# Kernel optimization log

Hardware: AMD Instinct MI355X
Metric: run time of the kernel (lower is better)

## Reference

```python
import jax, jax.numpy as jnp
import numpy as np

A = 64        # atom_fea_len
NBR = 41      # nbr_fea_len
ORIG = 92     # orig_atom_fea_len
NCONV = 3
N = 50000     # total atoms
M = 12        # neighbors per atom
B = 1000      # crystals
NPC = 50      # atoms per crystal (B*NPC == N)
EPS = 1e-5


def setup_inputs() -> dict:
    key = jax.random.key(0)
    ks = jax.random.split(key, 16)
    s = lambda k, shape: (jax.random.normal(k, shape, jnp.float32) * 0.05)
    inp = {
        "atom_fea": jax.random.normal(ks[0], (N, ORIG), jnp.float32),
        "nbr_fea": jax.random.uniform(ks[1], (N, M, NBR), dtype=jnp.float32),
        "nbr_fea_idx": jax.random.randint(ks[2], (N, M), 0, N),
        "crystal_atom_idx": jnp.arange(B * NPC).reshape(B, NPC),
        # params (weights stored as (in, out) so fwd is x @ w + b)
        "emb_w": s(ks[3], (ORIG, A)),
        "fc_full_w": s(ks[4], (NCONV, 2 * A + NBR, 2 * A)),
        "fc_full_b": s(ks[5], (NCONV, 2 * A)),
        "bn1_g": jnp.ones((NCONV, 2 * A), jnp.float32),
        "bn1_b": jnp.zeros((NCONV, 2 * A), jnp.float32),
        "bn2_g": jnp.ones((NCONV, A), jnp.float32),
        "bn2_b": jnp.zeros((NCONV, A), jnp.float32),
        "adj_w": s(ks[6], (6, A, A)),   # torch Bilinear weight (out, in1, in2)
        "adj_b": s(ks[7], (6,)),
        "fc1_w": s(ks[8], (6, 6)),
        "fc1_b": s(ks[9], (6,)),
        "af_w": s(ks[10], (A, ORIG)),
        "af_b": s(ks[11], (ORIG,)),
    }
    return inp


def _batchnorm(x, g, b):
    # training-mode BN over axis 0 (torch default biased variance)
    m = jnp.mean(x, axis=0)
    v = jnp.var(x, axis=0)
    return (x - m) * jax.lax.rsqrt(v + EPS) * g + b


def _conv_layer(x, nbr_fea, nbr_idx, w, b, g1, b1, g2, b2):
    n, m = nbr_idx.shape
    atom_nbr = x[nbr_idx]  # (N, M, A) gather
    total = jnp.concatenate(
        [jnp.broadcast_to(x[:, None, :], (n, m, A)), atom_nbr, nbr_fea], axis=2
    )  # (N, M, 2A+NBR)
    gated = total @ w + b  # (N, M, 2A)
    gated = _batchnorm(gated.reshape(-1, 2 * A), g1, b1).reshape(n, m, 2 * A)
    nbr_filter, nbr_core = gated[..., :A], gated[..., A:]
    summed = jnp.sum(jax.nn.sigmoid(nbr_filter) * jax.nn.softplus(nbr_core), axis=1)
    summed = _batchnorm(summed, g2, b2)
    return jax.nn.softplus(x + summed)


def reference(atom_fea, nbr_fea, nbr_fea_idx, crystal_atom_idx, emb_w,
              fc_full_w, fc_full_b, bn1_g, bn1_b, bn2_g, bn2_b,
              adj_w, adj_b, fc1_w, fc1_b, af_w, af_b):
    x = atom_fea @ emb_w  # embedding, no bias
    for i in range(NCONV):
        x = _conv_layer(x, nbr_fea, nbr_fea_idx,
                        fc_full_w[i], fc_full_b[i],
                        bn1_g[i], bn1_b[i], bn2_g[i], bn2_b[i])
    cf = x[crystal_atom_idx]  # (B, NPC, A)
    # Original code bug: fc_adj(x1, x2) is called with x1 == x2 == tiled atom
    # features, so pair (i, j) depends only on atom j. Compute per-atom bilinear
    # then tile -> identical output.
    q = jnp.einsum('bnd,ode,bne->bno', cf, adj_w, cf) + adj_b  # (B, NPC, 6)
    q = q @ fc1_w + fc1_b
    logp = jax.nn.log_softmax(q, axis=-1)  # row-wise over the 6 classes
    edge_prob = jnp.broadcast_to(logp[:, None, :, :], (B, NPC, NPC, 6)).reshape(B, NPC * NPC, 6)
    atom_feature = cf @ af_w + af_b  # (B, NPC, ORIG)
    return edge_prob, atom_feature
```

## Files before the change

### kernel.cpp

```cpp
#include <hip/hip_runtime.h>
#include <hip/hip_bf16.h>

#define AA 64
#define NBRF 41
#define ORIGD 92
#define NATOM 50000
#define MM 12
#define NB 1000
#define NPCC 50
#define NEDGE (NATOM*MM)
#define NREP 64
constexpr float EPS_BN = 1e-5f;

using bf16 = __hip_bfloat16;
typedef short s16x8 __attribute__((ext_vector_type(8)));
typedef float f32x4 __attribute__((ext_vector_type(4)));

__device__ __forceinline__ float u2f(unsigned short u) {
    union { float f; unsigned int i; } v; v.i = ((unsigned int)u) << 16; return v.f;
}
__device__ __forceinline__ unsigned short f2bu(float f) {
    bf16 h = __float2bfloat16(f);
    return *reinterpret_cast<unsigned short*>(&h);
}
__device__ __forceinline__ float fsigmoid(float x) {
    float e = __expf(-x);
    return __builtin_amdgcn_rcpf(1.f + e);
}
__device__ __forceinline__ float fsoftplus(float x) {
    return fmaxf(x, 0.f) + __logf(1.f + __expf(-fabsf(x)));
}

#define GLD16(g, l)                                                              \
    __builtin_amdgcn_global_load_lds(                                            \
        (const __attribute__((address_space(1))) unsigned int*)(g),              \
        (__attribute__((address_space(3))) unsigned int*)(l), 16, 0, 0)

__global__ __launch_bounds__(256) void k_prepN(const float* __restrict__ nf,
                                               unsigned short* __restrict__ nbp) {
    const int total = NEDGE * 6;
    for (int i = blockIdx.x * 256 + threadIdx.x; i < total; i += gridDim.x * 256) {
        int row = i / 6, j = i - row * 6;
        const float* src = nf + (size_t)row * NBRF + j * 8;
        int base = j * 8;
        unsigned short h[8];
        #pragma unroll
        for (int e = 0; e < 8; ++e)
            h[e] = (base + e < NBRF) ? f2bu(src[e]) : (unsigned short)0;
        uint4 u;
        u.x = (unsigned)h[0] | ((unsigned)h[1] << 16);
        u.y = (unsigned)h[2] | ((unsigned)h[3] << 16);
        u.z = (unsigned)h[4] | ((unsigned)h[5] << 16);
        u.w = (unsigned)h[6] | ((unsigned)h[7] << 16);
        *reinterpret_cast<uint4*>(nbp + (size_t)row * 48 + j * 8) = u;
    }
}

__global__ void k_prepW(const float* __restrict__ W_all, unsigned short* __restrict__ WtAll,
                        const float* __restrict__ adjw, unsigned short* __restrict__ Bq,
                        float* __restrict__ stats, int nstat) {
    int b = blockIdx.x, t = threadIdx.x;
    if (b < 9) {
        int layer = b / 3, part = b - layer * 3;
        const float* W = W_all + (size_t)layer * 169 * 128;
        unsigned short* Wt = WtAll + layer * 27648 + part * 9216;
        for (int i = t; i < 9216; i += 256) {
            int n = i / 72, k = i - n * 72;
            float v = 0.f;
            if (part == 0)      { if (k < NBRF) v = W[(128 + k) * 128 + n]; }
            else if (part == 1) { if (k < 64)   v = W[(64 + k) * 128 + n]; }
            else                { if (k < 64)   v = W[k * 128 + n]; }
            Wt[i] = f2bu(v);
        }
    } else if (b < 12) {
        int base = (b - 9) * 9216;
        for (int i = t; i < 9216; i += 256) {
            int idx = base + i;
            int n = idx / 72, k = idx - n * 72;
            float v = (k < 64) ? adjw[(n >> 6) * 4096 + k * 64 + (n & 63)] : 0.f;
            Bq[idx] = f2bu(v);
        }
    } else {
        int base = (b - 12) * 2048;
        for (int i = t; i < 2048; i += 256) {
            int idx = base + i;
            if (idx < nstat) stats[idx] = 0.f;
        }
    }
}

__global__ __launch_bounds__(256) void k_embed(const float* __restrict__ af,
                                               const float* __restrict__ w,
                                               unsigned short* __restrict__ xb) {
    __shared__ float wl[ORIGD * AA];
    __shared__ float al[4][ORIGD];
    int t = threadIdx.x;
    for (int i = t; i < ORIGD * AA; i += 256) wl[i] = w[i];
    int n0 = blockIdx.x * 4;
    for (int i = t; i < 4 * ORIGD; i += 256) {
        int a = i / ORIGD, k = i - a * ORIGD;
        al[a][k] = af[(size_t)(n0 + a) * ORIGD + k];
    }
    __syncthreads();
    int c = t & 63, a = t >> 6;
    float acc = 0.f;
    #pragma unroll 4
    for (int k = 0; k < ORIGD; ++k)
        acc += al[a][k] * wl[k * AA + c];
    xb[(size_t)(n0 + a) * AA + c] = f2bu(acc);
}

__global__ __launch_bounds__(256, 2) void k_passA(const unsigned short* __restrict__ xb,
                                                  const unsigned short* __restrict__ nbp,
                                                  const unsigned short* __restrict__ Wt,
                                                  const int* __restrict__ nidx,
                                                  float* __restrict__ stats,
                                                  uint4* __restrict__ gated) {
    __shared__ __attribute__((aligned(16))) unsigned char SMEM[63488];
    unsigned short* A   = reinterpret_cast<unsigned short*>(SMEM);
    unsigned short* As  = A + 192 * 64;
    unsigned short* Bl0 = As + 16 * 64;
    unsigned short* Bl1 = Bl0 + 128 * 72;
    int t = threadIdx.x;
    int n0 = blockIdx.x * 16;
    int w = t >> 6, lane = t & 63, ln = lane & 15, quad = lane >> 4;

    const unsigned short* nbrow = nbp + (size_t)n0 * MM * 48;
    for (int c = w; c < 18; c += 4)
        GLD16(nbrow + c * 512 + lane * 8, (char*)A + c * 1024);
    for (int c = w; c < 18; c += 4)
        GLD16(Wt + c * 512 + lane * 8, (char*)Bl0 + c * 1024);
    for (int c = w; c < 18; c += 4)
        GLD16(Wt + 9216 + c * 512 + lane * 8, (char*)Bl1 + c * 1024);
    int sl = ((lane & 7) ^ ((lane >> 3) & 7)) * 8;
    if (w == 3) {
        GLD16(xb + (size_t)(n0 + (lane >> 3)) * 64 + sl, (char*)As);
        GLD16(xb + (size_t)(n0 + 8 + (lane >> 3)) * 64 + sl, (char*)As + 1024);
    }
    if (t < 64) A[192 * 48 + t] = 0;
    const int* nb = nidx + n0 * MM;
    int idxv[6];
    #pragma unroll
    for (int c = 0; c < 6; ++c) idxv[c] = nb[w * 48 + c * 8 + (lane >> 3)];
    __syncthreads();

    f32x4 acc[3][8];
    f32x4 z4 = {0.f, 0.f, 0.f, 0.f};
    for (int i = 0; i < 3; ++i) for (int j = 0; j < 8; ++j) acc[i][j] = z4;
    int sw0 = (quad ^ (ln & 7)) * 8, sw1 = ((quad + 4) ^ (ln & 7)) * 8;

    #pragma unroll
    for (int mt = 0; mt < 3; ++mt) {
        int mrow = w * 48 + mt * 16 + ln;
        s16x8 a0 = *reinterpret_cast<const s16x8*>(&A[mrow * 48 + quad * 8]);
        s16x8 a1 = *reinterpret_cast<const s16x8*>(&A[mrow * 48 + quad * 8 + 32]);
        #pragma unroll
        for (int nt = 0; nt < 8; ++nt) {
            int nrow = nt * 16 + ln;
            s16x8 b0 = *reinterpret_cast<const s16x8*>(&Bl0[nrow * 72 + quad * 8]);
            s16x8 b1 = *reinterpret_cast<const s16x8*>(&Bl0[nrow * 72 + quad * 8 + 32]);
            acc[mt][nt] = __builtin_amdgcn_mfma_f32_16x16x32_bf16(a0, b0, acc[mt][nt], 0, 0, 0);
            acc[mt][nt] = __builtin_amdgcn_mfma_f32_16x16x32_bf16(a1, b1, acc[mt][nt], 0, 0, 0);
        }
    }
    __syncthreads();
    #pragma unroll
    for (int c = 0; c < 6; ++c)
        GLD16(xb + (size_t)idxv[c] * 64 + sl, (char*)A + (w * 48 + c * 8) * 128);
    for (int c = w; c < 18; c += 4)
        GLD16(Wt + 2 * 9216 + c * 512 + lane * 8, (char*)Bl0 + c * 1024);
    __syncthreads();

    #pragma unroll
    for (int mt = 0; mt < 3; ++mt) {
        int mrow = w * 48 + mt * 16 + ln;
        s16x8 a0 = *reinterpret_cast<const s16x8*>(&A[mrow * 64 + sw0]);
        s16x8 a1 = *reinterpret_cast<const s16x8*>(&A[mrow * 64 + sw1]);
        #pragma unroll
        for (int nt = 0; nt < 8; ++nt) {
            int nrow = nt * 16 + ln;
            s16x8 b0 = *reinterpret_cast<const s16x8*>(&Bl1[nrow * 72 + quad * 8]);
            s16x8 b1 = *reinterpret_cast<const s16x8*>(&Bl1[nrow * 72 + quad * 8 + 32]);
            acc[mt][nt] = __builtin_amdgcn_mfma_f32_16x16x32_bf16(a0, b0, acc[mt][nt], 0, 0, 0);
            acc[mt][nt] = __builtin_amdgcn_mfma_f32_16x16x32_bf16(a1, b1, acc[mt][nt], 0, 0, 0);
        }
    }
    #pragma unroll
    for (int mt = 0; mt < 3; ++mt) {
        int mrow = w * 48 + mt * 16 + ln;
        int atom = mrow / 12;
        int s0 = (quad ^ (atom & 7)) * 8, s1 = ((quad + 4) ^ (atom & 7)) * 8;
        s16x8 a0 = *reinterpret_cast<const s16x8*>(&As[atom * 64 + s0]);
        s16x8 a1 = *reinterpret_cast<const s16x8*>(&As[atom * 64 + s1]);
        #pragma unroll
        for (int nt = 0; nt < 8; ++nt) {
            int nrow = nt * 16 + ln;
            s16x8 b0 = *reinterpret_cast<const s16x8*>(&Bl0[nrow * 72 + quad * 8]);
            s16x8 b1 = *reinterpret_cast<const s16x8*>(&Bl0[nrow * 72 + quad * 8 + 32]);
            acc[mt][nt] = __builtin_amdgcn_mfma_f32_16x16x32_bf16(a0, b0, acc[mt][nt], 0, 0, 0);
            acc[mt][nt] = __builtin_amdgcn_mfma_f32_16x16x32_bf16(a1, b1, acc[mt][nt], 0, 0, 0);
        }
    }

    uint4* gblk = gated + (size_t)blockIdx.x * 3072;
    float s[8] = {0,0,0,0,0,0,0,0}, q[8] = {0,0,0,0,0,0,0,0};
    #pragma unroll
    for (int mt = 0; mt < 3; ++mt) {
        #pragma unroll
        for (int reg = 0; reg < 4; ++reg) {
            float r[8];
            #pragma unroll
            for (int nt = 0; nt < 8; ++nt) {
                r[nt] = acc[mt][nt][reg];
                s[nt] += r[nt]; q[nt] += r[nt] * r[nt];
            }
            uint4 u;
            u.x = (unsigned)f2bu(r[0]) | ((unsigned)f2bu(r[1]) << 16);
            u.y = (unsigned)f2bu(r[2]) | ((unsigned)f2bu(r[3]) << 16);
            u.z = (unsigned)f2bu(r[4]) | ((unsigned)f2bu(r[5]) << 16);
            u.w = (unsigned)f2bu(r[6]) | ((unsigned)f2bu(r[7]) << 16);
            gblk[(mt * 4 + reg) * 256 + t] = u;
        }
    }
    #pragma unroll
    for (int nt = 0; nt < 8; ++nt) {
        s[nt] += __shfl_xor(s[nt], 16); s[nt] += __shfl_xor(s[nt], 32);
        q[nt] += __shfl_xor(q[nt], 16); q[nt] += __shfl_xor(q[nt], 32);
    }
    __syncthreads();
    float* red = reinterpret_cast<float*>(SMEM);
    if (quad == 0) {
        #pragma unroll
        for (int nt = 0; nt < 8; ++nt) {
            red[((w * 8 + nt) * 16 + ln) * 2 + 0] = s[nt];
            red[((w * 8 + nt) * 16 + ln) * 2 + 1] = q[nt];
        }
    }
    __syncthreads();
    {
        int c = t >> 1, j = t & 1;
        float v = 0.f;
        #pragma unroll
        for (int w2 = 0; w2 < 4; ++w2)
            v += red[((w2 * 8 + (c >> 4)) * 16 + (c & 15)) * 2 + j];
        int rep = (blockIdx.x & (NREP - 1)) << 8;
        atomicAdd(&stats[rep + j * 128 + c], v);
    }
}

__global__ void k_sc1(const float* __restrict__ stats, const float* __restrict__ g,
                      const float* __restrict__ b, float* __restrict__ sc) {
    int c = threadIdx.x;
    float s = 0.f, q = 0.f;
    for (int r = 0; r < NREP; ++r) {
        s += stats[r * 256 + c];
        q += stats[r * 256 + 128 + c];
    }
    float cnt = (float)NEDGE;
    float mean = s / cnt;
    float var = q / cnt - mean * mean;
    float inv = rsqrtf(var + EPS_BN);
    float scale = g[c] * inv;
    sc[c] = scale;
    sc[128 + c] = b[c] - mean * scale;
}

__global__ __launch_bounds__(256) void k_passBs(const uint4* __restrict__ gated,
                                                const float* __restrict__ sc,
                                                float* __restrict__ summed,
                                                float* __restrict__ stats2,
                                                float* __restrict__ stats1z) {
    int t = threadIdx.x;
    if (blockIdx.x < 16) {
        int i0 = blockIdx.x * 1024;
        for (int i = t; i < 1024; i += 256) stats1z[i0 + i] = 0.f;
    }
    int n0 = blockIdx.x * 16;
    int w = t >> 6, lane = t & 63, ln = lane & 15, quad = lane >> 4;
    float scF[4], shF[4], scC[4], shC[4];
    #pragma unroll
    for (int nt = 0; nt < 4; ++nt) {
        int cc = nt * 16 + ln;
        scF[nt] = sc[cc];      shF[nt] = sc[128 + cc];
        scC[nt] = sc[64 + cc]; shC[nt] = sc[192 + cc];
    }
    const uint4* gblk = gated + (size_t)blockIdx.x * 3072;
    float bkt[3][4] = {{0,0,0,0},{0,0,0,0},{0,0,0,0}};
    #pragma unroll
    for (int mt = 0; mt < 3; ++mt) {
        #pragma unroll
        for (int reg = 0; reg < 4; ++reg) {
            uint4 u = gblk[(mt * 4 + reg) * 256 + t];
            unsigned uu[4] = {u.x, u.y, u.z, u.w};
            #pragma unroll
            for (int nt = 0; nt < 4; ++nt) {
                float rfv = u2f((unsigned short)((nt & 1) ? (uu[nt >> 1] >> 16) : (uu[nt >> 1] & 0xffff)));
                float rcv = u2f((unsigned short)((nt & 1) ? (uu[2 + (nt >> 1)] >> 16) : (uu[2 + (nt >> 1)] & 0xffff)));
                float rf = rfv * scF[nt] + shF[nt];
                float rc = rcv * scC[nt] + shC[nt];
                bkt[mt][nt] += fsigmoid(rf) * fsoftplus(rc);
            }
        }
    }
    float S0[4], S1[4], S2[4], S3[4];
    #pragma unroll
    for (int nt = 0; nt < 4; ++nt) {
        S0[nt] = (quad < 3) ? bkt[0][nt] : 0.f;
        S1[nt] = (quad <= 1) ? bkt[1][nt] : ((quad == 3) ? bkt[0][nt] : 0.f);
        S2[nt] = (quad == 0) ? bkt[2][nt] : ((quad >= 2) ? bkt[1][nt] : 0.f);
        S3[nt] = (quad >= 1) ? bkt[2][nt] : 0.f;
    }
    #pragma unroll
    for (int nt = 0; nt < 4; ++nt) {
        S0[nt] += __shfl_xor(S0[nt], 16); S0[nt] += __shfl_xor(S0[nt], 32);
        S1[nt] += __shfl_xor(S1[nt], 16); S1[nt] += __shfl_xor(S1[nt], 32);
        S2[nt] += __shfl_xor(S2[nt], 16); S2[nt] += __shfl_xor(S2[nt], 32);
        S3[nt] += __shfl_xor(S3[nt], 16); S3[nt] += __shfl_xor(S3[nt], 32);
    }
    #pragma unroll
    for (int nt = 0; nt < 4; ++nt) {
        float v = (quad == 0) ? S0[nt] : (quad == 1) ? S1[nt] : (quad == 2) ? S2[nt] : S3[nt];
        summed[(size_t)(n0 + w * 4 + quad) * AA + nt * 16 + ln] = v;
    }
    if (quad == 0) {
        int rep = ((blockIdx.x * 4 + w) & (NREP - 1)) << 7;
        #pragma unroll
        for (int nt = 0; nt < 4; ++nt) {
            float sA = S0[nt] + S1[nt] + S2[nt] + S3[nt];
            float qA = S0[nt]*S0[nt] + S1[nt]*S1[nt] + S2[nt]*S2[nt] + S3[nt]*S3[nt];
            atomicAdd(&stats2[rep + nt * 16 + ln], sA);
            atomicAdd(&stats2[rep + 64 + nt * 16 + ln], qA);
        }
    }
}

__global__ void k_sc2(const float* __restrict__ stats2, const float* __restrict__ g,
                      const float* __restrict__ b, float* __restrict__ sc2) {
    int c = threadIdx.x;
    float s = 0.f, q = 0.f;
    for (int r = 0; r < NREP; ++r) {
        s += stats2[r * 128 + c];
        q += stats2[r * 128 + 64 + c];
    }
    float cnt = (float)NATOM;
    float mean = s / cnt;
    float var = q / cnt - mean * mean;
    float inv = rsqrtf(var + EPS_BN);
    float scale = g[c] * inv;
    sc2[c] = scale;
    sc2[64 + c] = b[c] - mean * scale;
}

__global__ void k_update(unsigned short* __restrict__ xb, const float* __restrict__ summed,
                         const float* __restrict__ sc2, float* __restrict__ stats2z) {
    if (blockIdx.x < 8) {
        int i0 = blockIdx.x * 1024;
        for (int i = threadIdx.x; i < 1024; i += 256) stats2z[i0 + i] = 0.f;
    }
    int i = blockIdx.x * blockDim.x + threadIdx.x;
    if (i < NATOM * AA) {
        int c = i & 63;
        float s = summed[i] * sc2[c] + sc2[64 + c];
        xb[i] = f2bu(fsoftplus(u2f(xb[i]) + s));
    }
}

__global__ __launch_bounds__(256) void k_q(const unsigned short* __restrict__ xb,
                                           const int* __restrict__ cidx,
                                           const unsigned short* __restrict__ Bq,
                                           const float* __restrict__ adjb,
                                           const float* __restrict__ fc1w,
                                           const float* __restrict__ fc1b,
                                           float* __restrict__ logp) {
    __shared__ __attribute__((aligned(16))) unsigned short Aq[64 * 72];
    __shared__ __attribute__((aligned(16))) unsigned short Bl[384 * 72];
    __shared__ float qv[64][6];
    int t = threadIdx.x;
    for (int i = t; i < 3456; i += 256)
        reinterpret_cast<uint4*>(Bl)[i] = reinterpret_cast<const uint4*>(Bq)[i];

    int w = t >> 6, lane = t & 63, ln = lane & 15, quad = lane >> 4;
    float bo[6];
    #pragma unroll
    for (int o = 0; o < 6; ++o) bo[o] = adjb[o];

    for (int ch = 0; ch < 4; ++ch) {
        int p0 = blockIdx.x * 256 + ch * 64;
        __syncthreads();
        for (int i = t; i < 64 * 72; i += 256) {
            int a = i / 72, k = i - a * 72;
            int ga = p0 + a;
            Aq[i] = (k < 64 && ga < NATOM)
                ? xb[(size_t)cidx[ga < NATOM ? ga : 0] * AA + k] : (unsigned short)0;
        }
        __syncthreads();

        f32x4 acc[24];
        f32x4 z4 = {0.f, 0.f, 0.f, 0.f};
        #pragma unroll
        for (int i = 0; i < 24; ++i) acc[i] = z4;
        {
            int mrow = w * 16 + ln;
            s16x8 a0 = *reinterpret_cast<const s16x8*>(&Aq[mrow * 72 + quad * 8]);
            s16x8 a1 = *reinterpret_cast<const s16x8*>(&Aq[mrow * 72 + quad * 8 + 32]);
            #pragma unroll
            for (int nt = 0; nt < 24; ++nt) {
                int nrow = nt * 16 + ln;
                s16x8 b0 = *reinterpret_cast<const s16x8*>(&Bl[nrow * 72 + quad * 8]);
                s16x8 b1 = *reinterpret_cast<const s16x8*>(&Bl[nrow * 72 + quad * 8 + 32]);
                acc[nt] = __builtin_amdgcn_mfma_f32_16x16x32_bf16(a0, b0, acc[nt], 0, 0, 0);
                acc[nt] = __builtin_amdgcn_mfma_f32_16x16x32_bf16(a1, b1, acc[nt], 0, 0, 0);
            }
        }
        float cfv[4][4];
        #pragma unroll
        for (int reg = 0; reg < 4; ++reg) {
            int ga = p0 + w * 16 + quad * 4 + reg;
            const unsigned short* xr = xb + (size_t)cidx[ga < NATOM ? ga : 0] * AA;
            #pragma unroll
            for (int et = 0; et < 4; ++et)
                cfv[reg][et] = (ga < NATOM) ? u2f(xr[et * 16 + ln]) : 0.f;
        }
        #pragma unroll
        for (int reg = 0; reg < 4; ++reg) {
            #pragma unroll
            for (int o = 0; o < 6; ++o) {
                float p = 0.f;
                #pragma unroll
                for (int et = 0; et < 4; ++et)
                    p += acc[o * 4 + et][reg] * cfv[reg][et];
                p += __shfl_xor(p, 1); p += __shfl_xor(p, 2);
                p += __shfl_xor(p, 4); p += __shfl_xor(p, 8);
                if (ln == 0) qv[w * 16 + quad * 4 + reg][o] = p + bo[o];
            }
        }
        __syncthreads();
        if (t < 64) {
            int ga = p0 + t;
            if (ga < NATOM) {
                float q2[6];
                float mx = -1e30f;
                #pragma unroll
                for (int o2 = 0; o2 < 6; ++o2) {
                    float acc2 = fc1b[o2];
                    #pragma unroll
                    for (int o = 0; o < 6; ++o) acc2 += qv[t][o] * fc1w[o * 6 + o2];
                    q2[o2] = acc2; mx = fmaxf(mx, acc2);
                }
                float se = 0.f;
                #pragma unroll
                for (int o2 = 0; o2 < 6; ++o2) se += __expf(q2[o2] - mx);
                float lse = mx + __logf(se);
                #pragma unroll
                for (int o2 = 0; o2 < 6; ++o2) logp[(size_t)ga * 6 + o2] = q2[o2] - lse;
            }
        }
    }
}

__global__ void k_edge(const float* __restrict__ logp, float* __restrict__ out0) {
    int i4 = blockIdx.x * blockDim.x + threadIdx.x;
    if (i4 >= (NB * NPCC * NPCC * 6) / 4) return;
    int e = i4 * 4;
    int b = e / (NPCC * NPCC * 6);
    int rr = e - b * (NPCC * NPCC * 6);
    const float* lb = &logp[(size_t)b * NPCC * 6];
    float4 v;
    int r0 = rr % 300;       v.x = lb[r0];
    int r1 = (rr + 1) % 300; v.y = lb[r1];
    int r2 = (rr + 2) % 300; v.z = lb[r2];
    int r3 = (rr + 3) % 300; v.w = lb[r3];
    *reinterpret_cast<float4*>(&out0[e]) = v;
}

__global__ __launch_bounds__(256) void k_af(const unsigned short* __restrict__ xb,
                                            const int* __restrict__ cidx,
                                            const float* __restrict__ afw,
                                            const float* __restrict__ afb,
                                            float* __restrict__ out1) {
    __shared__ float wl[AA * ORIGD];
    __shared__ float cfl[64][AA];
    __shared__ float bl[ORIGD];
    int t = threadIdx.x;
    for (int i = t; i < AA * ORIGD; i += 256) wl[i] = afw[i];
    if (t < ORIGD) bl[t] = afb[t];
    int p0 = blockIdx.x * 64;
    for (int i = t; i < 64 * AA; i += 256) {
        int a = i >> 6, e = i & 63;
        int ga = p0 + a;
        cfl[a][e] = (ga < NATOM) ? u2f(xb[(size_t)cidx[ga] * AA + e]) : 0.f;
    }
    __syncthreads();
    for (int i = t; i < 64 * ORIGD; i += 256) {
        int a = i / ORIGD, c = i - a * ORIGD;
        int ga = p0 + a;
        if (ga < NATOM) {
            float acc = bl[c];
            #pragma unroll 8
            for (int k = 0; k < AA; ++k)
                acc += cfl[a][k] * wl[k * ORIGD + c];
            out1[(size_t)ga * ORIGD + c] = acc;
        }
    }
}

extern "C" void kernel_launch(void* const* d_in, const int* in_sizes, int n_in,
                              void* d_out, int out_size, void* d_ws, size_t ws_size,
                              hipStream_t stream) {
    (void)in_sizes; (void)n_in; (void)out_size; (void)ws_size;
    const float* atom_fea  = (const float*)d_in[0];
    const float* nbr_fea   = (const float*)d_in[1];
    const int*   nbr_idx   = (const int*)d_in[2];
    const int*   cidx      = (const int*)d_in[3];
    const float* emb_w     = (const float*)d_in[4];
    const float* fc_full_w = (const float*)d_in[5];
    const float* bn1_g = (const float*)d_in[7];
    const float* bn1_b = (const float*)d_in[8];
    const float* bn2_g = (const float*)d_in[9];
    const float* bn2_b = (const float*)d_in[10];
    const float* adj_w = (const float*)d_in[11];
    const float* adj_b = (const float*)d_in[12];
    const float* fc1_w = (const float*)d_in[13];
    const float* fc1_b = (const float*)d_in[14];
    const float* af_w  = (const float*)d_in[15];
    const float* af_b  = (const float*)d_in[16];

    float* out0 = (float*)d_out;
    float* out1 = out0 + (size_t)NB * NPCC * NPCC * 6;

    float* ws = (float*)d_ws;
    float* summed = ws;
    float* logp   = summed + (size_t)NATOM * AA;
    float* stats1 = logp + (size_t)NATOM * 6;
    float* stats2 = stats1 + (size_t)NREP * 256;
    float* sc1    = stats2 + (size_t)NREP * 128;
    float* sc2    = sc1 + 256;
    float* endf   = sc2 + 128;
    size_t off = (((size_t)((char*)endf - (char*)d_ws)) + 255) & ~(size_t)255;
    unsigned short* xb    = (unsigned short*)((char*)d_ws + off);
    unsigned short* WtAll = xb + (size_t)NATOM * 64;
    unsigned short* Bq    = WtAll + 3 * 27648;
    unsigned short* nbp   = Bq + 384 * 72;
    size_t goff = (off + ((size_t)NATOM * 64 + 3 * 27648 + 384 * 72 + (size_t)NEDGE * 48) * 2 + 255) & ~(size_t)255;
    uint4* gated = (uint4*)((char*)d_ws + goff);

    const int nstat = NREP * 256 + NREP * 128;
    k_prepN<<<2048, 256, 0, stream>>>(nbr_fea, nbp);
    k_prepW<<<24, 256, 0, stream>>>(fc_full_w, WtAll, adj_w, Bq, stats1, nstat);
    k_embed<<<NATOM / 4, 256, 0, stream>>>(atom_fea, emb_w, xb);
    for (int layer = 0; layer < 3; ++layer) {
        const unsigned short* Wt = WtAll + layer * 27648;
        k_passA<<<NATOM / 16, 256, 0, stream>>>(xb, nbp, Wt, nbr_idx, stats1, gated);
        k_sc1<<<1, 128, 0, stream>>>(stats1, bn1_g + layer * 128, bn1_b + layer * 128, sc1);
        k_passBs<<<NATOM / 16, 256, 0, stream>>>(gated, sc1, summed, stats2, stats1);
        k_sc2<<<1, 64, 0, stream>>>(stats2, bn2_g + layer * 64, bn2_b + layer * 64, sc2);
        k_update<<<(NATOM * AA + 255) / 256, 256, 0, stream>>>(xb, summed, sc2, stats2);
    }
    k_q<<<(NATOM + 255) / 256, 256, 0, stream>>>(xb, cidx, Bq, adj_b, fc1_w, fc1_b, logp);
    k_edge<<<((NB * NPCC * NPCC * 6) / 4 + 255) / 256, 256, 0, stream>>>(logp, out0);
    k_af<<<(NATOM + 63) / 64, 256, 0, stream>>>(xb, cidx, af_w, af_b, out1);
}
```

Baseline: 723.1 us.

## Recompute gated GEMM in second pass instead of storing bf16 intermediates

Pass A now only accumulates the batch-norm statistics and no longer writes the bf16 gated tensor. A new pass B re-stages the inputs, recomputes the same MFMA GEMM, then applies BN1, the sigmoid·softplus gating and the neighbor sum. This trades the write and read of a large (N·M·128) bf16 intermediate for doubled matrix-core work and gather traffic. The final q kernel is also changed to use one 64-atom chunk per block instead of four, giving more blocks.

Result: slower. 774.2 us (+7.1%).

```diff
diff --git a/kernel.cpp b/kernel.cpp
--- a/kernel.cpp
+++ b/kernel.cpp
@@ -110,118 +110,106 @@
     xb[(size_t)(n0 + a) * AA + c] = f2bu(acc);
 }
 
+#define PASS_STAGE_AND_MFMA(xb, nbp, Wt, nidx)                                        \
+    unsigned short* A   = reinterpret_cast<unsigned short*>(SMEM);                    \
+    unsigned short* As  = A + 192 * 64;                                               \
+    unsigned short* Bl0 = As + 16 * 64;                                               \
+    unsigned short* Bl1 = Bl0 + 128 * 72;                                             \
+    const unsigned short* nbrow = nbp + (size_t)n0 * MM * 48;                         \
+    for (int c = w; c < 18; c += 4)                                                   \
+        GLD16(nbrow + c * 512 + lane * 8, (char*)A + c * 1024);                       \
+    for (int c = w; c < 18; c += 4)                                                   \
+        GLD16(Wt + c * 512 + lane * 8, (char*)Bl0 + c * 1024);                        \
+    for (int c = w; c < 18; c += 4)                                                   \
+        GLD16(Wt + 9216 + c * 512 + lane * 8, (char*)Bl1 + c * 1024);                 \
+    int sl = ((lane & 7) ^ ((lane >> 3) & 7)) * 8;                                    \
+    if (w == 3) {                                                                     \
+        GLD16(xb + (size_t)(n0 + (lane >> 3)) * 64 + sl, (char*)As);                  \
+        GLD16(xb + (size_t)(n0 + 8 + (lane >> 3)) * 64 + sl, (char*)As + 1024);       \
+    }                                                                                 \
+    if (t < 64) A[192 * 48 + t] = 0;  \
+    const int* nb = nidx + n0 * MM;                                                   \
+    int idxv[6];                                                                      \
+    _Pragma("unroll")                                                                 \
+    for (int c = 0; c < 6; ++c) idxv[c] = nb[w * 48 + c * 8 + (lane >> 3)];           \
+    __syncthreads();                                                                  \
+    f32x4 acc[3][8];                                                                  \
+    { f32x4 z4 = {0.f, 0.f, 0.f, 0.f};                                                \
+      for (int i = 0; i < 3; ++i) for (int j = 0; j < 8; ++j) acc[i][j] = z4; }       \
+    int sw0 = (quad ^ (ln & 7)) * 8, sw1 = ((quad + 4) ^ (ln & 7)) * 8;               \
+    _Pragma("unroll")                                                                 \
+    for (int mt = 0; mt < 3; ++mt) {                                                  \
+        int mrow = w * 48 + mt * 16 + ln;                                             \
+        s16x8 a0 = *reinterpret_cast<const s16x8*>(&A[mrow * 48 + quad * 8]);         \
+        s16x8 a1 = *reinterpret_cast<const s16x8*>(&A[mrow * 48 + quad * 8 + 32]);    \
+        _Pragma("unroll")                                                             \
+        for (int nt = 0; nt < 8; ++nt) {                                              \
+            int nrow = nt * 16 + ln;                                                  \
+            s16x8 b0 = *reinterpret_cast<const s16x8*>(&Bl0[nrow * 72 + quad * 8]);   \
+            s16x8 b1 = *reinterpret_cast<const s16x8*>(&Bl0[nrow * 72 + quad * 8 + 32]); \
+            acc[mt][nt] = __builtin_amdgcn_mfma_f32_16x16x32_bf16(a0, b0, acc[mt][nt], 0, 0, 0); \
+            acc[mt][nt] = __builtin_amdgcn_mfma_f32_16x16x32_bf16(a1, b1, acc[mt][nt], 0, 0, 0); \
+        }                                                                             \
+    }                                                                                 \
+    __syncthreads();                                                                  \
+    _Pragma("unroll")                                                                 \
+    for (int c = 0; c < 6; ++c)                                                       \
+        GLD16(xb + (size_t)idxv[c] * 64 + sl, (char*)A + (w * 48 + c * 8) * 128);     \
+    for (int c = w; c < 18; c += 4)                                                   \
+        GLD16(Wt + 2 * 9216 + c * 512 + lane * 8, (char*)Bl0 + c * 1024);             \
+    __syncthreads();                                                                  \
+    _Pragma("unroll")                                                                 \
+    for (int mt = 0; mt < 3; ++mt) {                                                  \
+        int mrow = w * 48 + mt * 16 + ln;                                             \
+        s16x8 a0 = *reinterpret_cast<const s16x8*>(&A[mrow * 64 + sw0]);              \
+        s16x8 a1 = *reinterpret_cast<const s16x8*>(&A[mrow * 64 + sw1]);              \
+        _Pragma("unroll")                                                             \
+        for (int nt = 0; nt < 8; ++nt) {                                              \
+            int nrow = nt * 16 + ln;                                                  \
+            s16x8 b0 = *reinterpret_cast<const s16x8*>(&Bl1[nrow * 72 + quad * 8]);   \
+            s16x8 b1 = *reinterpret_cast<const s16x8*>(&Bl1[nrow * 72 + quad * 8 + 32]); \
+            acc[mt][nt] = __builtin_amdgcn_mfma_f32_16x16x32_bf16(a0, b0, acc[mt][nt], 0, 0, 0); \
+            acc[mt][nt] = __builtin_amdgcn_mfma_f32_16x16x32_bf16(a1, b1, acc[mt][nt], 0, 0, 0); \
+        }                                                                             \
+    }                                                                                 \
+    _Pragma("unroll")                                                                 \
+    for (int mt = 0; mt < 3; ++mt) {                                                  \
+        int mrow = w * 48 + mt * 16 + ln;                                             \
+        int atom = mrow / 12;                                                         \
+        int s0 = (quad ^ (atom & 7)) * 8, s1 = ((quad + 4) ^ (atom & 7)) * 8;         \
+        s16x8 a0 = *reinterpret_cast<const s16x8*>(&As[atom * 64 + s0]);              \
+        s16x8 a1 = *reinterpret_cast<const s16x8*>(&As[atom * 64 + s1]);              \
+        _Pragma("unroll")                                                             \
+        for (int nt = 0; nt < 8; ++nt) {                                              \
+            int nrow = nt * 16 + ln;                                                  \
+            s16x8 b0 = *reinterpret_cast<const s16x8*>(&Bl0[nrow * 72 + quad * 8]);   \
+            s16x8 b1 = *reinterpret_cast<const s16x8*>(&Bl0[nrow * 72 + quad * 8 + 32]); \
+            acc[mt][nt] = __builtin_amdgcn_mfma_f32_16x16x32_bf16(a0, b0, acc[mt][nt], 0, 0, 0); \
+            acc[mt][nt] = __builtin_amdgcn_mfma_f32_16x16x32_bf16(a1, b1, acc[mt][nt], 0, 0, 0); \
+        }                                                                             \
+    }
+
 __global__ __launch_bounds__(256, 2) void k_passA(const unsigned short* __restrict__ xb,
                                                   const unsigned short* __restrict__ nbp,
                                                   const unsigned short* __restrict__ Wt,
                                                   const int* __restrict__ nidx,
-                                                  float* __restrict__ stats,
-                                                  uint4* __restrict__ gated) {
+                                                  float* __restrict__ stats) {
     __shared__ __attribute__((aligned(16))) unsigned char SMEM[63488];
-    unsigned short* A   = reinterpret_cast<unsigned short*>(SMEM);
-    unsigned short* As  = A + 192 * 64;
-    unsigned short* Bl0 = As + 16 * 64;
-    unsigned short* Bl1 = Bl0 + 128 * 72;
     int t = threadIdx.x;
     int n0 = blockIdx.x * 16;
     int w = t >> 6, lane = t & 63, ln = lane & 15, quad = lane >> 4;
-
-    const unsigned short* nbrow = nbp + (size_t)n0 * MM * 48;
-    for (int c = w; c < 18; c += 4)
-        GLD16(nbrow + c * 512 + lane * 8, (char*)A + c * 1024);
-    for (int c = w; c < 18; c += 4)
-        GLD16(Wt + c * 512 + lane * 8, (char*)Bl0 + c * 1024);
-    for (int c = w; c < 18; c += 4)
-        GLD16(Wt + 9216 + c * 512 + lane * 8, (char*)Bl1 + c * 1024);
-    int sl = ((lane & 7) ^ ((lane >> 3) & 7)) * 8;
-    if (w == 3) {
-        GLD16(xb + (size_t)(n0 + (lane >> 3)) * 64 + sl, (char*)As);
-        GLD16(xb + (size_t)(n0 + 8 + (lane >> 3)) * 64 + sl, (char*)As + 1024);
-    }
-    if (t < 64) A[192 * 48 + t] = 0;
-    const int* nb = nidx + n0 * MM;
-    int idxv[6];
-    #pragma unroll
-    for (int c = 0; c < 6; ++c) idxv[c] = nb[w * 48 + c * 8 + (lane >> 3)];
-    __syncthreads();
-
-    f32x4 acc[3][8];
-    f32x4 z4 = {0.f, 0.f, 0.f, 0.f};
-    for (int i = 0; i < 3; ++i) for (int j = 0; j < 8; ++j) acc[i][j] = z4;
-    int sw0 = (quad ^ (ln & 7)) * 8, sw1 = ((quad + 4) ^ (ln & 7)) * 8;
-
-    #pragma unroll
-    for (int mt = 0; mt < 3; ++mt) {
-        int mrow = w * 48 + mt * 16 + ln;
-        s16x8 a0 = *reinterpret_cast<const s16x8*>(&A[mrow * 48 + quad * 8]);
-        s16x8 a1 = *reinterpret_cast<const s16x8*>(&A[mrow * 48 + quad * 8 + 32]);
-        #pragma unroll
-        for (int nt = 0; nt < 8; ++nt) {
-            int nrow = nt * 16 + ln;
-            s16x8 b0 = *reinterpret_cast<const s16x8*>(&Bl0[nrow * 72 + quad * 8]);
-            s16x8 b1 = *reinterpret_cast<const s16x8*>(&Bl0[nrow * 72 + quad * 8 + 32]);
-            acc[mt][nt] = __builtin_amdgcn_mfma_f32_16x16x32_bf16(a0, b0, acc[mt][nt], 0, 0, 0);
-            acc[mt][nt] = __builtin_amdgcn_mfma_f32_16x16x32_bf16(a1, b1, acc[mt][nt], 0, 0, 0);
-        }
-    }
-    __syncthreads();
-    #pragma unroll
-    for (int c = 0; c < 6; ++c)
-        GLD16(xb + (size_t)idxv[c] * 64 + sl, (char*)A + (w * 48 + c * 8) * 128);
-    for (int c = w; c < 18; c += 4)
-        GLD16(Wt + 2 * 9216 + c * 512 + lane * 8, (char*)Bl0 + c * 1024);
-    __syncthreads();
-
-    #pragma unroll
-    for (int mt = 0; mt < 3; ++mt) {
-        int mrow = w * 48 + mt * 16 + ln;
-        s16x8 a0 = *reinterpret_cast<const s16x8*>(&A[mrow * 64 + sw0]);
-        s16x8 a1 = *reinterpret_cast<const s16x8*>(&A[mrow * 64 + sw1]);
-        #pragma unroll
-        for (int nt = 0; nt < 8; ++nt) {
-            int nrow = nt * 16 + ln;
-            s16x8 b0 = *reinterpret_cast<const s16x8*>(&Bl1[nrow * 72 + quad * 8]);
-            s16x8 b1 = *reinterpret_cast<const s16x8*>(&Bl1[nrow * 72 + quad * 8 + 32]);
-            acc[mt][nt] = __builtin_amdgcn_mfma_f32_16x16x32_bf16(a0, b0, acc[mt][nt], 0, 0, 0);
-            acc[mt][nt] = __builtin_amdgcn_mfma_f32_16x16x32_bf16(a1, b1, acc[mt][nt], 0, 0, 0);
-        }
-    }
-    #pragma unroll
-    for (int mt = 0; mt < 3; ++mt) {
-        int mrow = w * 48 + mt * 16 + ln;
-        int atom = mrow / 12;
-        int s0 = (quad ^ (atom & 7)) * 8, s1 = ((quad + 4) ^ (atom & 7)) * 8;
-        s16x8 a0 = *reinterpret_cast<const s16x8*>(&As[atom * 64 + s0]);
-        s16x8 a1 = *reinterpret_cast<const s16x8*>(&As[atom * 64 + s1]);
-        #pragma unroll
-        for (int nt = 0; nt < 8; ++nt) {
-            int nrow = nt * 16 + ln;
-            s16x8 b0 = *reinterpret_cast<const s16x8*>(&Bl0[nrow * 72 + quad * 8]);
-            s16x8 b1 = *reinterpret_cast<const s16x8*>(&Bl0[nrow * 72 + quad * 8 + 32]);
-            acc[mt][nt] = __builtin_amdgcn_mfma_f32_16x16x32_bf16(a0, b0, acc[mt][nt], 0, 0, 0);
-            acc[mt][nt] = __builtin_amdgcn_mfma_f32_16x16x32_bf16(a1, b1, acc[mt][nt], 0, 0, 0);
-        }
-    }
-
-    uint4* gblk = gated + (size_t)blockIdx.x * 3072;
+    PASS_STAGE_AND_MFMA(xb, nbp, Wt, nidx)
+
     float s[8] = {0,0,0,0,0,0,0,0}, q[8] = {0,0,0,0,0,0,0,0};
     #pragma unroll
-    for (int mt = 0; mt < 3; ++mt) {
-        #pragma unroll
-        for (int reg = 0; reg < 4; ++reg) {
-            float r[8];
+    for (int mt = 0; mt < 3; ++mt)
+        #pragma unroll
+        for (int reg = 0; reg < 4; ++reg)
             #pragma unroll
             for (int nt = 0; nt < 8; ++nt) {
-                r[nt] = acc[mt][nt][reg];
-                s[nt] += r[nt]; q[nt] += r[nt] * r[nt];
+                float r = acc[mt][nt][reg];
+                s[nt] += r; q[nt] += r * r;
             }
-            uint4 u;
-            u.x = (unsigned)f2bu(r[0]) | ((unsigned)f2bu(r[1]) << 16);
-            u.y = (unsigned)f2bu(r[2]) | ((unsigned)f2bu(r[3]) << 16);
-            u.z = (unsigned)f2bu(r[4]) | ((unsigned)f2bu(r[5]) << 16);
-            u.w = (unsigned)f2bu(r[6]) | ((unsigned)f2bu(r[7]) << 16);
-            gblk[(mt * 4 + reg) * 256 + t] = u;
-        }
-    }
     #pragma unroll
     for (int nt = 0; nt < 8; ++nt) {
         s[nt] += __shfl_xor(s[nt], 16); s[nt] += __shfl_xor(s[nt], 32);
@@ -245,6 +233,74 @@
             v += red[((w2 * 8 + (c >> 4)) * 16 + (c & 15)) * 2 + j];
         int rep = (blockIdx.x & (NREP - 1)) << 8;
         atomicAdd(&stats[rep + j * 128 + c], v);
+    }
+}
+
+__global__ __launch_bounds__(256, 2) void k_passB(const unsigned short* __restrict__ xb,
+                                                  const unsigned short* __restrict__ nbp,
+                                                  const unsigned short* __restrict__ Wt,
+                                                  const int* __restrict__ nidx,
+                                                  const float* __restrict__ sc,
+                                                  float* __restrict__ summed,
+                                                  float* __restrict__ stats2,
+                                                  float* __restrict__ stats1z) {
+    __shared__ __attribute__((aligned(16))) unsigned char SMEM[63488];
+    int t = threadIdx.x;
+    if (blockIdx.x < 16) {
+        int i0 = blockIdx.x * 1024;
+        for (int i = t; i < 1024; i += 256) stats1z[i0 + i] = 0.f;
+    }
+    int n0 = blockIdx.x * 16;
+    int w = t >> 6, lane = t & 63, ln = lane & 15, quad = lane >> 4;
+    PASS_STAGE_AND_MFMA(xb, nbp, Wt, nidx)
+
+    float scF[4], shF[4], scC[4], shC[4];
+    #pragma unroll
+    for (int nt = 0; nt < 4; ++nt) {
+        int cc = nt * 16 + ln;
+        scF[nt] = sc[cc];      shF[nt] = sc[128 + cc];
+        scC[nt] = sc[64 + cc]; shC[nt] = sc[192 + cc];
+    }
+    float bkt[3][4] = {{0,0,0,0},{0,0,0,0},{0,0,0,0}};
+    #pragma unroll
+    for (int mt = 0; mt < 3; ++mt)
+        #pragma unroll
+        for (int reg = 0; reg < 4; ++reg)
+            #pragma unroll
+            for (int nt = 0; nt < 4; ++nt) {
+                float rf = acc[mt][nt][reg]     * scF[nt] + shF[nt];
+                float rc = acc[mt][nt + 4][reg] * scC[nt] + shC[nt];
+                bkt[mt][nt] += fsigmoid(rf) * fsoftplus(rc);
+            }
+    float S0[4], S1[4], S2[4], S3[4];
+    #pragma unroll
+    for (int nt = 0; nt < 4; ++nt) {
+        S0[nt] = (quad < 3) ? bkt[0][nt] : 0.f;
+        S1[nt] = (quad <= 1) ? bkt[1][nt] : ((quad == 3) ? bkt[0][nt] : 0.f);
+        S2[nt] = (quad == 0) ? bkt[2][nt] : ((quad >= 2) ? bkt[1][nt] : 0.f);
+        S3[nt] = (quad >= 1) ? bkt[2][nt] : 0.f;
+    }
+    #pragma unroll
+    for (int nt = 0; nt < 4; ++nt) {
+        S0[nt] += __shfl_xor(S0[nt], 16); S0[nt] += __shfl_xor(S0[nt], 32);
+        S1[nt] += __shfl_xor(S1[nt], 16); S1[nt] += __shfl_xor(S1[nt], 32);
+        S2[nt] += __shfl_xor(S2[nt], 16); S2[nt] += __shfl_xor(S2[nt], 32);
+        S3[nt] += __shfl_xor(S3[nt], 16); S3[nt] += __shfl_xor(S3[nt], 32);
+    }
+    #pragma unroll
+    for (int nt = 0; nt < 4; ++nt) {
+        float v = (quad == 0) ? S0[nt] : (quad == 1) ? S1[nt] : (quad == 2) ? S2[nt] : S3[nt];
+        summed[(size_t)(n0 + w * 4 + quad) * AA + nt * 16 + ln] = v;
+    }
+    if (quad == 0) {
+        int rep = ((blockIdx.x * 4 + w) & (NREP - 1)) << 7;
+        #pragma unroll
+        for (int nt = 0; nt < 4; ++nt) {
+            float sA = S0[nt] + S1[nt] + S2[nt] + S3[nt];
+            float qA = S0[nt]*S0[nt] + S1[nt]*S1[nt] + S2[nt]*S2[nt] + S3[nt]*S3[nt];
+            atomicAdd(&stats2[rep + nt * 16 + ln], sA);
+            atomicAdd(&stats2[rep + 64 + nt * 16 + ln], qA);
+        }
     }
 }
 
@@ -263,75 +319,6 @@
     float scale = g[c] * inv;
     sc[c] = scale;
     sc[128 + c] = b[c] - mean * scale;
-}
-
-__global__ __launch_bounds__(256) void k_passBs(const uint4* __restrict__ gated,
-                                                const float* __restrict__ sc,
-                                                float* __restrict__ summed,
-                                                float* __restrict__ stats2,
-                                                float* __restrict__ stats1z) {
-    int t = threadIdx.x;
-    if (blockIdx.x < 16) {
-        int i0 = blockIdx.x * 1024;
-        for (int i = t; i < 1024; i += 256) stats1z[i0 + i] = 0.f;
-    }
-    int n0 = blockIdx.x * 16;
-    int w = t >> 6, lane = t & 63, ln = lane & 15, quad = lane >> 4;
-    float scF[4], shF[4], scC[4], shC[4];
-    #pragma unroll
-    for (int nt = 0; nt < 4; ++nt) {
-        int cc = nt * 16 + ln;
-        scF[nt] = sc[cc];      shF[nt] = sc[128 + cc];
-        scC[nt] = sc[64 + cc]; shC[nt] = sc[192 + cc];
-    }
-    const uint4* gblk = gated + (size_t)blockIdx.x * 3072;
-    float bkt[3][4] = {{0,0,0,0},{0,0,0,0},{0,0,0,0}};
-    #pragma unroll
-    for (int mt = 0; mt < 3; ++mt) {
-        #pragma unroll
-        for (int reg = 0; reg < 4; ++reg) {
-            uint4 u = gblk[(mt * 4 + reg) * 256 + t];
-            unsigned uu[4] = {u.x, u.y, u.z, u.w};
-            #pragma unroll
-            for (int nt = 0; nt < 4; ++nt) {
-                float rfv = u2f((unsigned short)((nt & 1) ? (uu[nt >> 1] >> 16) : (uu[nt >> 1] & 0xffff)));
-                float rcv = u2f((unsigned short)((nt & 1) ? (uu[2 + (nt >> 1)] >> 16) : (uu[2 + (nt >> 1)] & 0xffff)));
-                float rf = rfv * scF[nt] + shF[nt];
-                float rc = rcv * scC[nt] + shC[nt];
-                bkt[mt][nt] += fsigmoid(rf) * fsoftplus(rc);
-            }
-        }
-    }
-    float S0[4], S1[4], S2[4], S3[4];
-    #pragma unroll
-    for (int nt = 0; nt < 4; ++nt) {
-        S0[nt] = (quad < 3) ? bkt[0][nt] : 0.f;
-        S1[nt] = (quad <= 1) ? bkt[1][nt] : ((quad == 3) ? bkt[0][nt] : 0.f);
-        S2[nt] = (quad == 0) ? bkt[2][nt] : ((quad >= 2) ? bkt[1][nt] : 0.f);
-        S3[nt] = (quad >= 1) ? bkt[2][nt] : 0.f;
-    }
-    #pragma unroll
-    for (int nt = 0; nt < 4; ++nt) {
-        S0[nt] += __shfl_xor(S0[nt], 16); S0[nt] += __shfl_xor(S0[nt], 32);
-        S1[nt] += __shfl_xor(S1[nt], 16); S1[nt] += __shfl_xor(S1[nt], 32);
-        S2[nt] += __shfl_xor(S2[nt], 16); S2[nt] += __shfl_xor(S2[nt], 32);
-        S3[nt] += __shfl_xor(S3[nt], 16); S3[nt] += __shfl_xor(S3[nt], 32);
-    }
-    #pragma unroll
-    for (int nt = 0; nt < 4; ++nt) {
-        float v = (quad == 0) ? S0[nt] : (quad == 1) ? S1[nt] : (quad == 2) ? S2[nt] : S3[nt];
-        summed[(size_t)(n0 + w * 4 + quad) * AA + nt * 16 + ln] = v;
-    }
-    if (quad == 0) {
-        int rep = ((blockIdx.x * 4 + w) & (NREP - 1)) << 7;
-        #pragma unroll
-        for (int nt = 0; nt < 4; ++nt) {
-            float sA = S0[nt] + S1[nt] + S2[nt] + S3[nt];
-            float qA = S0[nt]*S0[nt] + S1[nt]*S1[nt] + S2[nt]*S2[nt] + S3[nt]*S3[nt];
-            atomicAdd(&stats2[rep + nt * 16 + ln], sA);
-            atomicAdd(&stats2[rep + 64 + nt * 16 + ln], qA);
-        }
-    }
 }
 
 __global__ void k_sc2(const float* __restrict__ stats2, const float* __restrict__ g,
@@ -376,84 +363,79 @@
     __shared__ __attribute__((aligned(16))) unsigned short Bl[384 * 72];
     __shared__ float qv[64][6];
     int t = threadIdx.x;
+    int p0 = blockIdx.x * 64;
+    for (int i = t; i < 64 * 72; i += 256) {
+        int a = i / 72, k = i - a * 72;
+        int ga = p0 + a;
+        Aq[i] = (k < 64 && ga < NATOM)
+            ? xb[(size_t)cidx[ga < NATOM ? ga : 0] * AA + k] : (unsigned short)0;
+    }
     for (int i = t; i < 3456; i += 256)
         reinterpret_cast<uint4*>(Bl)[i] = reinterpret_cast<const uint4*>(Bq)[i];
+    __syncthreads();
 
     int w = t >> 6, lane = t & 63, ln = lane & 15, quad = lane >> 4;
+    f32x4 acc[24];
+    f32x4 z4 = {0.f, 0.f, 0.f, 0.f};
+    #pragma unroll
+    for (int i = 0; i < 24; ++i) acc[i] = z4;
+    {
+        int mrow = w * 16 + ln;
+        s16x8 a0 = *reinterpret_cast<const s16x8*>(&Aq[mrow * 72 + quad * 8]);
+        s16x8 a1 = *reinterpret_cast<const s16x8*>(&Aq[mrow * 72 + quad * 8 + 32]);
+        #pragma unroll
+        for (int nt = 0; nt < 24; ++nt) {
+            int nrow = nt * 16 + ln;
+            s16x8 b0 = *reinterpret_cast<const s16x8*>(&Bl[nrow * 72 + quad * 8]);
+            s16x8 b1 = *reinterpret_cast<const s16x8*>(&Bl[nrow * 72 + quad * 8 + 32]);
+            acc[nt] = __builtin_amdgcn_mfma_f32_16x16x32_bf16(a0, b0, acc[nt], 0, 0, 0);
+            acc[nt] = __builtin_amdgcn_mfma_f32_16x16x32_bf16(a1, b1, acc[nt], 0, 0, 0);
+        }
+    }
+    float cfv[4][4];
+    #pragma unroll
+    for (int reg = 0; reg < 4; ++reg) {
+        int ga = p0 + w * 16 + quad * 4 + reg;
+        const unsigned short* xr = xb + (size_t)cidx[ga < NATOM ? ga : 0] * AA;
+        #pragma unroll
+        for (int et = 0; et < 4; ++et)
+            cfv[reg][et] = (ga < NATOM) ? u2f(xr[et * 16 + ln]) : 0.f;
+    }
     float bo[6];
     #pragma unroll
     for (int o = 0; o < 6; ++o) bo[o] = adjb[o];
-
-    for (int ch = 0; ch < 4; ++ch) {
-        int p0 = blockIdx.x * 256 + ch * 64;
-        __syncthreads();
-        for (int i = t; i < 64 * 72; i += 256) {
-            int a = i / 72, k = i - a * 72;
-            int ga = p0 + a;
-            Aq[i] = (k < 64 && ga < NATOM)
-                ? xb[(size_t)cidx[ga < NATOM ? ga : 0] * AA + k] : (unsigned short)0;
-        }
-        __syncthreads();
-
-        f32x4 acc[24];
-        f32x4 z4 = {0.f, 0.f, 0.f, 0.f};
-        #pragma unroll
-        for (int i = 0; i < 24; ++i) acc[i] = z4;
-        {
-            int mrow = w * 16 + ln;
-            s16x8 a0 = *reinterpret_cast<const s16x8*>(&Aq[mrow * 72 + quad * 8]);
-            s16x8 a1 = *reinterpret_cast<const s16x8*>(&Aq[mrow * 72 + quad * 8 + 32]);
-            #pragma unroll
-            for (int nt = 0; nt < 24; ++nt) {
-                int nrow = nt * 16 + ln;
-                s16x8 b0 = *reinterpret_cast<const s16x8*>(&Bl[nrow * 72 + quad * 8]);
-                s16x8 b1 = *reinterpret_cast<const s16x8*>(&Bl[nrow * 72 + quad * 8 + 32]);
-                acc[nt] = __builtin_amdgcn_mfma_f32_16x16x32_bf16(a0, b0, acc[nt], 0, 0, 0);
-                acc[nt] = __builtin_amdgcn_mfma_f32_16x16x32_bf16(a1, b1, acc[nt], 0, 0, 0);
-            }
-        }
-        float cfv[4][4];
-        #pragma unroll
-        for (int reg = 0; reg < 4; ++reg) {
-            int ga = p0 + w * 16 + quad * 4 + reg;
-            const unsigned short* xr = xb + (size_t)cidx[ga < NATOM ? ga : 0] * AA;
+    #pragma unroll
+    for (int reg = 0; reg < 4; ++reg) {
+        #pragma unroll
+        for (int o = 0; o < 6; ++o) {
+            float p = 0.f;
             #pragma unroll
             for (int et = 0; et < 4; ++et)
-                cfv[reg][et] = (ga < NATOM) ? u2f(xr[et * 16 + ln]) : 0.f;
-        }
-        #pragma unroll
-        for (int reg = 0; reg < 4; ++reg) {
+                p += acc[o * 4 + et][reg] * cfv[reg][et];
+            p += __shfl_xor(p, 1); p += __shfl_xor(p, 2);
+            p += __shfl_xor(p, 4); p += __shfl_xor(p, 8);
+            if (ln == 0) qv[w * 16 + quad * 4 + reg][o] = p + bo[o];
+        }
+    }
+    __syncthreads();
+    if (t < 64) {
+        int ga = p0 + t;
+        if (ga < NATOM) {
+            float q2[6];
+            float mx = -1e30f;
             #pragma unroll
-            for (int o = 0; o < 6; ++o) {
-                float p = 0.f;
+            for (int o2 = 0; o2 < 6; ++o2) {
+                float acc2 = fc1b[o2];
                 #pragma unroll
-                for (int et = 0; et < 4; ++et)
-                    p += acc[o * 4 + et][reg] * cfv[reg][et];
-                p += __shfl_xor(p, 1); p += __shfl_xor(p, 2);
-                p += __shfl_xor(p, 4); p += __shfl_xor(p, 8);
-                if (ln == 0) qv[w * 16 + quad * 4 + reg][o] = p + bo[o];
+                for (int o = 0; o < 6; ++o) acc2 += qv[t][o] * fc1w[o * 6 + o2];
+                q2[o2] = acc2; mx = fmaxf(mx, acc2);
             }
-        }
-        __syncthreads();
-        if (t < 64) {
-            int ga = p0 + t;
-            if (ga < NATOM) {
-                float q2[6];
-                float mx = -1e30f;
-                #pragma unroll
-                for (int o2 = 0; o2 < 6; ++o2) {
-                    float acc2 = fc1b[o2];
-                    #pragma unroll
-                    for (int o = 0; o < 6; ++o) acc2 += qv[t][o] * fc1w[o * 6 + o2];
-                    q2[o2] = acc2; mx = fmaxf(mx, acc2);
-                }
-                float se = 0.f;
-                #pragma unroll
-                for (int o2 = 0; o2 < 6; ++o2) se += __expf(q2[o2] - mx);
-                float lse = mx + __logf(se);
-                #pragma unroll
-                for (int o2 = 0; o2 < 6; ++o2) logp[(size_t)ga * 6 + o2] = q2[o2] - lse;
-            }
+            float se = 0.f;
+            #pragma unroll
+            for (int o2 = 0; o2 < 6; ++o2) se += __expf(q2[o2] - mx);
+            float lse = mx + __logf(se);
+            #pragma unroll
+            for (int o2 = 0; o2 < 6; ++o2) logp[(size_t)ga * 6 + o2] = q2[o2] - lse;
         }
     }
 }
@@ -541,8 +523,6 @@
     unsigned short* WtAll = xb + (size_t)NATOM * 64;
     unsigned short* Bq    = WtAll + 3 * 27648;
     unsigned short* nbp   = Bq + 384 * 72;
-    size_t goff = (off + ((size_t)NATOM * 64 + 3 * 27648 + 384 * 72 + (size_t)NEDGE * 48) * 2 + 255) & ~(size_t)255;
-    uint4* gated = (uint4*)((char*)d_ws + goff);
 
     const int nstat = NREP * 256 + NREP * 128;
     k_prepN<<<2048, 256, 0, stream>>>(nbr_fea, nbp);
@@ -550,13 +530,13 @@
     k_embed<<<NATOM / 4, 256, 0, stream>>>(atom_fea, emb_w, xb);
     for (int layer = 0; layer < 3; ++layer) {
         const unsigned short* Wt = WtAll + layer * 27648;
-        k_passA<<<NATOM / 16, 256, 0, stream>>>(xb, nbp, Wt, nbr_idx, stats1, gated);
+        k_passA<<<NATOM / 16, 256, 0, stream>>>(xb, nbp, Wt, nbr_idx, stats1);
         k_sc1<<<1, 128, 0, stream>>>(stats1, bn1_g + layer * 128, bn1_b + layer * 128, sc1);
-        k_passBs<<<NATOM / 16, 256, 0, stream>>>(gated, sc1, summed, stats2, stats1);
+        k_passB<<<NATOM / 16, 256, 0, stream>>>(xb, nbp, Wt, nbr_idx, sc1, summed, stats2, stats1);
         k_sc2<<<1, 64, 0, stream>>>(stats2, bn2_g + layer * 64, bn2_b + layer * 64, sc2);
         k_update<<<(NATOM * AA + 255) / 256, 256, 0, stream>>>(xb, summed, sc2, stats2);
     }
-    k_q<<<(NATOM + 255) / 256, 256, 0, stream>>>(xb, cidx, Bq, adj_b, fc1_w, fc1_b, logp);
+    k_q<<<(NATOM + 63) / 64, 256, 0, stream>>>(xb, cidx, Bq, adj_b, fc1_w, fc1_b, logp);
     k_edge<<<((NB * NPCC * NPCC * 6) / 4 + 255) / 256, 256, 0, stream>>>(logp, out0);
     k_af<<<(NATOM + 63) / 64, 256, 0, stream>>>(xb, cidx, af_w, af_b, out1);
 }
```
